# Kernel optimization log

Measured on AMD Instinct MI355X. Metric: run time of the kernel, lower is better.

The kernel has to match this reference:

```python
import jax, jax.numpy as jnp
import numpy as np

D_MODEL = 1024
N_HEADS = 16
DEPTH = D_MODEL // N_HEADS


def setup_inputs() -> dict:
    key = jax.random.key(0)
    ks = jax.random.split(key, 11)
    B, S = 2, 2048
    s = 1.0 / np.sqrt(D_MODEL)
    return {
        "query": jax.random.normal(ks[0], (B, S, D_MODEL), jnp.float32),
        "key": jax.random.normal(ks[1], (B, S, D_MODEL), jnp.float32),
        "value": jax.random.normal(ks[2], (B, S, D_MODEL), jnp.float32),
        "Wq": jax.random.normal(ks[3], (D_MODEL, D_MODEL), jnp.float32) * s,
        "bq": jnp.zeros((D_MODEL,), jnp.float32),
        "Wk": jax.random.normal(ks[4], (D_MODEL, D_MODEL), jnp.float32) * s,
        "bk": jnp.zeros((D_MODEL,), jnp.float32),
        "Wv": jax.random.normal(ks[5], (D_MODEL, D_MODEL), jnp.float32) * s,
        "bv": jnp.zeros((D_MODEL,), jnp.float32),
        "Wo": jax.random.normal(ks[6], (D_MODEL, D_MODEL), jnp.float32) * s,
        "bo": jnp.zeros((D_MODEL,), jnp.float32),
    }


def _split_heads(x):
    B, S, _ = x.shape
    return x.reshape(B, S, N_HEADS, DEPTH).transpose(0, 2, 1, 3)  # [B,H,S,depth]


def reference(query, key, value, Wq, bq, Wk, bk, Wv, bv, Wo, bo):
    q = _split_heads(query @ Wq.T + bq)   # [B,H,S,d]
    k = _split_heads(key @ Wk.T + bk)
    v = _split_heads(value @ Wv.T + bv)
    scale = 1.0 / jnp.sqrt(jnp.asarray(DEPTH, jnp.float32))
    scores = jnp.einsum('bhqd,bhkd->bhqk', q, k) * scale  # [B,H,S,S]
    attn = jax.nn.softmax(scores, axis=-1)
    ctx = jnp.einsum('bhqk,bhkd->bhqd', attn, v)          # [B,H,S,d]
    B, H, S, d = ctx.shape
    ctx = ctx.transpose(0, 2, 1, 3).reshape(B, S, D_MODEL)
    out = ctx @ Wo.T + bo
    return out, attn
```

## Files before the change

### kernel.cpp

```cpp
#include <hip/hip_runtime.h>
#include <stdint.h>


#define DEV __device__ __forceinline__

typedef __attribute__((ext_vector_type(8))) short short8;
typedef __attribute__((ext_vector_type(4))) short short4v;
typedef __attribute__((ext_vector_type(4))) float f32x4;
typedef __attribute__((ext_vector_type(4))) uint32_t u32x4;

DEV short f2bf(float f) {
  uint32_t u = __builtin_bit_cast(uint32_t, f);
  u += 0x7fffu + ((u >> 16) & 1u);
  return (short)(u >> 16);
}

DEV uint32_t cvtpk_bf16(float a, float b) {
  uint32_t r;
  asm("v_cvt_pk_bf16_f32 %0, %1, %2" : "=v"(r) : "v"(a), "v"(b));
  return r;
}

DEV void gload_lds16(const void* g, void* l) {
  __builtin_amdgcn_global_load_lds(
      (const __attribute__((address_space(1))) void*)g,
      (__attribute__((address_space(3))) void*)l,
      16, 0, 0);
}

__global__ __launch_bounds__(256) void attn_fused(
    const short* __restrict__ q, const short* __restrict__ k,
    const short* __restrict__ vT, float* __restrict__ attn,
    short* __restrict__ ctx) {
  __shared__ __align__(16) char Ps[4 * 32 * 128];

  const int tid = threadIdx.x;
  const int lane = tid & 63;
  const int wm = tid >> 6;
  const int c = lane & 15;
  const int g = lane >> 4;
  const int orig = blockIdx.x;
  const int sid = (orig & 7) * 64 + (orig >> 3);
  const int qb = sid & 15;
  const int z = sid >> 4;

  const short* qz = q + (size_t)z * 131072 + (size_t)(qb * 128 + wm * 32) * 64;
  const short* kz = k + (size_t)z * 131072;
  const short* vz = vT + (size_t)z * 131072;
  float* az = attn + (size_t)z * 4194304 + (size_t)(qb * 128 + wm * 32) * 2048;

  short8 qf[2][2];
#pragma unroll
  for (int m = 0; m < 2; ++m)
#pragma unroll
    for (int kk = 0; kk < 2; ++kk)
      qf[m][kk] = *(const short8*)(qz + (m * 16 + c) * 64 + kk * 32 + g * 8);

  float l_part[2][4];
#pragma unroll
  for (int m = 0; m < 2; ++m)
#pragma unroll
    for (int j = 0; j < 4; ++j) l_part[m][j] = 0.f;

  for (int kt = 0; kt < 16; ++kt) {
    const short* kzt = kz + kt * 8192;
    f32x4 s[2][8];
#pragma unroll
    for (int m = 0; m < 2; ++m)
#pragma unroll
      for (int n = 0; n < 8; ++n) s[m][n] = f32x4{0.f, 0.f, 0.f, 0.f};
#pragma unroll
    for (int kk = 0; kk < 2; ++kk) {
#pragma unroll
      for (int n = 0; n < 8; ++n) {
        const short8 bf =
            *(const short8*)(kzt + (n * 16 + c) * 64 + kk * 32 + g * 8);
        s[0][n] = __builtin_amdgcn_mfma_f32_16x16x32_bf16(qf[0][kk], bf,
                                                          s[0][n], 0, 0, 0);
        s[1][n] = __builtin_amdgcn_mfma_f32_16x16x32_bf16(qf[1][kk], bf,
                                                          s[1][n], 0, 0, 0);
      }
    }
#pragma unroll
    for (int m = 0; m < 2; ++m)
#pragma unroll
      for (int j = 0; j < 4; ++j)
#pragma unroll
        for (int n = 0; n < 8; ++n) l_part[m][j] += __expf(s[m][n][j]);
  }

  float inv_l[2][4];
#pragma unroll
  for (int m = 0; m < 2; ++m)
#pragma unroll
    for (int j = 0; j < 4; ++j) {
      float l = l_part[m][j];
      l += __shfl_xor(l, 1, 64);
      l += __shfl_xor(l, 2, 64);
      l += __shfl_xor(l, 4, 64);
      l += __shfl_xor(l, 8, 64);
      inv_l[m][j] = 1.0f / l;
    }

  f32x4 o[2][4];
#pragma unroll
  for (int m = 0; m < 2; ++m)
#pragma unroll
    for (int n = 0; n < 4; ++n) o[m][n] = f32x4{0.f, 0.f, 0.f, 0.f};

  char* Pw = Ps + wm * 4096;

  for (int kt = 0; kt < 16; ++kt) {
    const short* kzt = kz + kt * 8192;
    f32x4 s[2][8];
#pragma unroll
    for (int m = 0; m < 2; ++m)
#pragma unroll
      for (int n = 0; n < 8; ++n) s[m][n] = f32x4{0.f, 0.f, 0.f, 0.f};
#pragma unroll
    for (int kk = 0; kk < 2; ++kk) {
#pragma unroll
      for (int n = 0; n < 8; ++n) {
        const short8 bf =
            *(const short8*)(kzt + (n * 16 + c) * 64 + kk * 32 + g * 8);
        s[0][n] = __builtin_amdgcn_mfma_f32_16x16x32_bf16(qf[0][kk], bf,
                                                          s[0][n], 0, 0, 0);
        s[1][n] = __builtin_amdgcn_mfma_f32_16x16x32_bf16(qf[1][kk], bf,
                                                          s[1][n], 0, 0, 0);
      }
    }
#pragma unroll
    for (int m = 0; m < 2; ++m)
#pragma unroll
      for (int j = 0; j < 4; ++j) {
        const float il = inv_l[m][j];
#pragma unroll
        for (int n = 0; n < 8; ++n) s[m][n][j] = __expf(s[m][n][j]) * il;
      }
#pragma unroll
    for (int m = 0; m < 2; ++m)
#pragma unroll
      for (int n = 0; n < 8; ++n)
#pragma unroll
        for (int j = 0; j < 4; ++j)
          __builtin_nontemporal_store(
              s[m][n][j], az + (size_t)(m * 16 + g * 4 + j) * 2048 +
                              kt * 128 + n * 16 + c);
#pragma unroll
    for (int kc = 0; kc < 4; ++kc) {
#pragma unroll
      for (int m = 0; m < 2; ++m)
#pragma unroll
        for (int nn = 0; nn < 2; ++nn)
#pragma unroll
          for (int j = 0; j < 4; ++j) {
            const int r = m * 16 + g * 4 + j;
            *(float*)(Pw + r * 128 +
                      (((nn * 16 + c) * 4) ^ ((r & 7) << 4))) =
                s[m][kc * 2 + nn][j];
          }
      short8 paf[2];
#pragma unroll
      for (int m = 0; m < 2; ++m) {
        const int r = m * 16 + c;
        const int X = (r & 7) << 4;
        const f32x4 lo = *(const f32x4*)(Pw + r * 128 + ((g * 32) ^ X));
        const f32x4 hi = *(const f32x4*)(Pw + r * 128 + ((g * 32 + 16) ^ X));
        u32x4 pk;
        pk[0] = cvtpk_bf16(lo[0], lo[1]);
        pk[1] = cvtpk_bf16(lo[2], lo[3]);
        pk[2] = cvtpk_bf16(hi[0], hi[1]);
        pk[3] = cvtpk_bf16(hi[2], hi[3]);
        paf[m] = __builtin_bit_cast(short8, pk);
      }
#pragma unroll
      for (int n2 = 0; n2 < 4; ++n2) {
        const short8 vf = *(const short8*)(vz + (size_t)(n2 * 16 + c) * 2048 +
                                           kt * 128 + kc * 32 + g * 8);
        o[0][n2] = __builtin_amdgcn_mfma_f32_16x16x32_bf16(paf[0], vf,
                                                           o[0][n2], 0, 0, 0);
        o[1][n2] = __builtin_amdgcn_mfma_f32_16x16x32_bf16(paf[1], vf,
                                                           o[1][n2], 0, 0, 0);
      }
    }
  }

  const int b = z >> 4, h = z & 15;
#pragma unroll
  for (int m = 0; m < 2; ++m)
#pragma unroll
    for (int n2 = 0; n2 < 4; ++n2)
#pragma unroll
      for (int j = 0; j < 4; ++j)
        ctx[((size_t)(b * 2048 + qb * 128 + wm * 32 + m * 16 + g * 4 + j)) *
                1024 + h * 64 + n2 * 16 + c] = f2bf(o[m][n2][j]);
}

enum { M_PROJ = 0, M_OUT = 3 };

struct GP {
  const void* A0; const void* A1; const void* A2;
  const short* B;
  const float* b0; const float* b1; const float* b2;
  void* C;
  int lda, ldb, K;
  long aBS, bBS;
};

template<int WM, int WN, int AM, int AN, bool CONVA, int MODE>
__global__ __launch_bounds__(256) void gemm_nt(GP p) {
  constexpr int BM = WM * 16 * AM;
  constexpr int BN = WN * 16 * AN;
  static_assert(WM * WN == 4, "4 waves / 256 threads");
  __shared__ __align__(16) char As[BM * 128];
  __shared__ __align__(16) char Bs[BN * 128];

  const int tid = threadIdx.x;
  const int lane = tid & 63;
  const int z = blockIdx.y;
  const int orig = blockIdx.x;
  const int sid = (orig & 7) * 32 + (orig >> 3);
  const int bm0 = (sid >> 3) * BM;
  const int bn0 = (sid & 7) * BN;

  const void* Aroot; const float* bias;
  if constexpr (MODE == M_PROJ) {
    Aroot = (z == 0) ? p.A0 : (z == 1 ? p.A1 : p.A2);
    bias  = (z == 0) ? p.b0 : (z == 1 ? p.b1 : p.b2);
  } else {
    Aroot = p.A0; bias = p.b0;
  }

  f32x4 acc[AM][AN];
#pragma unroll
  for (int m = 0; m < AM; ++m)
#pragma unroll
    for (int n = 0; n < AN; ++n) acc[m][n] = f32x4{0.f, 0.f, 0.f, 0.f};

  const int wave = tid >> 6;
  const int wm = wave / WN;
  const int wn = wave % WN;

  const int nK = p.K >> 6;
  for (int kt = 0; kt < nK; ++kt) {
    if constexpr (CONVA) {
      const float* Af = (const float*)Aroot + (size_t)z * p.aBS +
                        (size_t)bm0 * p.lda + kt * 64;
#pragma unroll
      for (int sw = 0; sw < BM / 16; ++sw) {
        const int r = sw * 16 + (tid >> 4);
        const int s8 = tid & 15;
        const float4 v = *(const float4*)(Af + (size_t)r * p.lda + s8 * 4);
        short4v oo;
        oo[0] = f2bf(v.x); oo[1] = f2bf(v.y); oo[2] = f2bf(v.z); oo[3] = f2bf(v.w);
        const int boff = (r * 128 + s8 * 8) ^ ((r & 7) << 4);
        *(short4v*)(As + boff) = oo;
      }
    } else {
      const short* Ab = (const short*)Aroot + (size_t)z * p.aBS +
                        (size_t)bm0 * p.lda + kt * 64;
#pragma unroll
      for (int sw = 0; sw < BM / 32; ++sw) {
        const int r = sw * 32 + (tid >> 3);
        const int c8 = (tid & 7) ^ (r & 7);
        gload_lds16(Ab + (size_t)r * p.lda + c8 * 8, As + (sw * 256 + tid) * 16);
      }
    }
    {
      const short* Bb = p.B + (size_t)z * p.bBS + (size_t)bn0 * p.ldb + kt * 64;
#pragma unroll
      for (int sw = 0; sw < BN / 32; ++sw) {
        const int r = sw * 32 + (tid >> 3);
        const int c8 = (tid & 7) ^ (r & 7);
        gload_lds16(Bb + (size_t)r * p.ldb + c8 * 8, Bs + (sw * 256 + tid) * 16);
      }
    }
    __syncthreads();
#pragma unroll
    for (int kk = 0; kk < 2; ++kk) {
      const int kb = kk * 64 + (lane >> 4) * 16;
      short8 aF[AM], bF[AN];
#pragma unroll
      for (int m = 0; m < AM; ++m) {
        const int r = wm * (16 * AM) + m * 16 + (lane & 15);
        aF[m] = *(const short8*)(As + ((r * 128 + kb) ^ ((r & 7) << 4)));
      }
#pragma unroll
      for (int n = 0; n < AN; ++n) {
        const int r = wn * (16 * AN) + n * 16 + (lane & 15);
        bF[n] = *(const short8*)(Bs + ((r * 128 + kb) ^ ((r & 7) << 4)));
      }
#pragma unroll
      for (int m = 0; m < AM; ++m)
#pragma unroll
        for (int n = 0; n < AN; ++n)
          acc[m][n] = __builtin_amdgcn_mfma_f32_16x16x32_bf16(
              aF[m], bF[n], acc[m][n], 0, 0, 0);
    }
    __syncthreads();
  }

#pragma unroll
  for (int m = 0; m < AM; ++m) {
#pragma unroll
    for (int n = 0; n < AN; ++n) {
#pragma unroll
      for (int j = 0; j < 4; ++j) {
        const int gm = bm0 + wm * (16 * AM) + m * 16 + ((lane >> 4) << 2) + j;
        const int gn = bn0 + wn * (16 * AN) + n * 16 + (lane & 15);
        const float v = acc[m][n][j];
        if constexpr (MODE == M_PROJ) {
          float vb = v + bias[gn];
          if (z == 0) vb *= 0.125f;
          const int b = gm >> 11, s = gm & 2047;
          const int h = gn >> 6, d = gn & 63;
          short* C = (short*)p.C;
          if (z < 2) {
            C[(size_t)z * 4194304 + (((size_t)(b * 16 + h) * 2048 + s) * 64 + d)] = f2bf(vb);
          } else {
            C[(size_t)2 * 4194304 + (((size_t)(b * 16 + h) * 64 + d) * 2048 + s)] = f2bf(vb);
          }
        } else {
          __builtin_nontemporal_store(
              v + bias[gn], (float*)p.C + (size_t)gm * 1024 + gn);
        }
      }
    }
  }
}

__global__ __launch_bounds__(256) void cvt_w(const float* w0, const float* w1,
                                             const float* w2, const float* w3,
                                             short* out) {
  const float* w = (blockIdx.y == 0) ? w0 : (blockIdx.y == 1) ? w1
                 : (blockIdx.y == 2) ? w2 : w3;
  short* o = out + (size_t)blockIdx.y * 1048576;
  const int i = (blockIdx.x * 256 + threadIdx.x) * 4;
  const float4 v = *(const float4*)(w + i);
  short4v s;
  s[0] = f2bf(v.x); s[1] = f2bf(v.y); s[2] = f2bf(v.z); s[3] = f2bf(v.w);
  *(short4v*)(o + i) = s;
}

extern "C" void kernel_launch(void* const* d_in, const int* in_sizes, int n_in,
                              void* d_out, int out_size, void* d_ws, size_t ws_size,
                              hipStream_t stream) {
  const float* query = (const float*)d_in[0];
  const float* key_  = (const float*)d_in[1];
  const float* value = (const float*)d_in[2];
  const float* Wq = (const float*)d_in[3];
  const float* bq = (const float*)d_in[4];
  const float* Wk = (const float*)d_in[5];
  const float* bk = (const float*)d_in[6];
  const float* Wv = (const float*)d_in[7];
  const float* bv = (const float*)d_in[8];
  const float* Wo = (const float*)d_in[9];
  const float* bo = (const float*)d_in[10];

  float* out  = (float*)d_out;
  float* attn = (float*)d_out + 4194304;

  short* ws   = (short*)d_ws;
  short* Wb   = ws;
  short* qkv  = ws + 4194304;
  short* ctx  = ws + 4 * 4194304;

  cvt_w<<<dim3(1024, 4), 256, 0, stream>>>(Wq, Wk, Wv, Wo, Wb);

  {
    GP p{};
    p.A0 = query; p.A1 = key_; p.A2 = value;
    p.B = Wb; p.b0 = bq; p.b1 = bk; p.b2 = bv;
    p.C = qkv;
    p.lda = 1024; p.ldb = 1024; p.K = 1024;
    p.aBS = 0; p.bBS = 1048576;
    gemm_nt<2, 2, 4, 4, true, M_PROJ><<<dim3(256, 3), 256, 0, stream>>>(p);
  }

  attn_fused<<<dim3(512), 256, 0, stream>>>(
      qkv, qkv + 4194304, qkv + 2 * 4194304, attn, ctx);

  {
    GP p{};
    p.A0 = ctx;
    p.B = Wb + 3 * 1048576;
    p.b0 = bo;
    p.C = out;
    p.lda = 1024; p.ldb = 1024; p.K = 1024;
    p.aBS = 0; p.bBS = 0;
    gemm_nt<2, 2, 4, 4, false, M_OUT><<<dim3(256, 1), 256, 0, stream>>>(p);
  }
}
```

Measured before the change: 315.6 us.

## Stage K/V tiles in LDS, vectorize attn stores, pre-convert activations to bf16

The attention kernel now stages each K tile (and the V^T tile) into swizzled shared memory with async global-to-LDS loads, so the four waves share them instead of each reading from global memory. Barriers are added around each tile. The attention-probability stores move to after the LDS transpose so they go out as 16-byte nontemporal vector stores rather than scalar stores. When the workspace is large enough, a new pre-pass converts the query, key and value activations to bf16 so the projection GEMM can skip in-loop fp32 conversion, at the cost of an extra read and write pass over the activations.

```diff
diff --git a/kernel.cpp b/kernel.cpp
--- a/kernel.cpp
+++ b/kernel.cpp
@@ -28,10 +28,27 @@
       16, 0, 0);
 }
 
+template<int UNITS, int SPR>
+DEV void stage_swz(const short* src, int stride, char* lds, int tid) {
+#pragma unroll
+  for (int i = 0; i < UNITS; ++i) {
+    const int u = tid + i * 256;
+    const int r = u / SPR;
+    const int s = (u % SPR) ^ (r & 7);
+    gload_lds16(src + (size_t)r * stride + s * 8, lds + u * 16);
+  }
+}
+
+DEV short8 ldsfrag(const char* lds, int row, int kbyte, int rowb) {
+  return *(const short8*)(lds + row * rowb + (kbyte ^ ((row & 7) << 4)));
+}
+
 __global__ __launch_bounds__(256) void attn_fused(
     const short* __restrict__ q, const short* __restrict__ k,
     const short* __restrict__ vT, float* __restrict__ attn,
     short* __restrict__ ctx) {
+  __shared__ __align__(16) char Ks[128 * 128];
+  __shared__ __align__(16) char Vs[64 * 256];
   __shared__ __align__(16) char Ps[4 * 32 * 128];
 
   const int tid = threadIdx.x;
@@ -63,7 +80,9 @@
     for (int j = 0; j < 4; ++j) l_part[m][j] = 0.f;
 
   for (int kt = 0; kt < 16; ++kt) {
-    const short* kzt = kz + kt * 8192;
+    if (kt) __syncthreads();
+    stage_swz<4, 8>(kz + kt * 8192, 64, Ks, tid);
+    __syncthreads();
     f32x4 s[2][8];
 #pragma unroll
     for (int m = 0; m < 2; ++m)
@@ -73,8 +92,7 @@
     for (int kk = 0; kk < 2; ++kk) {
 #pragma unroll
       for (int n = 0; n < 8; ++n) {
-        const short8 bf =
-            *(const short8*)(kzt + (n * 16 + c) * 64 + kk * 32 + g * 8);
+        const short8 bf = ldsfrag(Ks, n * 16 + c, kk * 64 + g * 16, 128);
         s[0][n] = __builtin_amdgcn_mfma_f32_16x16x32_bf16(qf[0][kk], bf,
                                                           s[0][n], 0, 0, 0);
         s[1][n] = __builtin_amdgcn_mfma_f32_16x16x32_bf16(qf[1][kk], bf,
@@ -111,7 +129,10 @@
   char* Pw = Ps + wm * 4096;
 
   for (int kt = 0; kt < 16; ++kt) {
-    const short* kzt = kz + kt * 8192;
+    __syncthreads();
+    stage_swz<4, 8>(kz + kt * 8192, 64, Ks, tid);
+    stage_swz<4, 16>(vz + kt * 128, 2048, Vs, tid);
+    __syncthreads();
     f32x4 s[2][8];
 #pragma unroll
     for (int m = 0; m < 2; ++m)
@@ -121,8 +142,7 @@
     for (int kk = 0; kk < 2; ++kk) {
 #pragma unroll
       for (int n = 0; n < 8; ++n) {
-        const short8 bf =
-            *(const short8*)(kzt + (n * 16 + c) * 64 + kk * 32 + g * 8);
+        const short8 bf = ldsfrag(Ks, n * 16 + c, kk * 64 + g * 16, 128);
         s[0][n] = __builtin_amdgcn_mfma_f32_16x16x32_bf16(qf[0][kk], bf,
                                                           s[0][n], 0, 0, 0);
         s[1][n] = __builtin_amdgcn_mfma_f32_16x16x32_bf16(qf[1][kk], bf,
@@ -137,15 +157,6 @@
 #pragma unroll
         for (int n = 0; n < 8; ++n) s[m][n][j] = __expf(s[m][n][j]) * il;
       }
-#pragma unroll
-    for (int m = 0; m < 2; ++m)
-#pragma unroll
-      for (int n = 0; n < 8; ++n)
-#pragma unroll
-        for (int j = 0; j < 4; ++j)
-          __builtin_nontemporal_store(
-              s[m][n][j], az + (size_t)(m * 16 + g * 4 + j) * 2048 +
-                              kt * 128 + n * 16 + c);
 #pragma unroll
     for (int kc = 0; kc < 4; ++kc) {
 #pragma unroll
@@ -166,6 +177,9 @@
         const int X = (r & 7) << 4;
         const f32x4 lo = *(const f32x4*)(Pw + r * 128 + ((g * 32) ^ X));
         const f32x4 hi = *(const f32x4*)(Pw + r * 128 + ((g * 32 + 16) ^ X));
+        float* dst = az + (size_t)r * 2048 + kt * 128 + kc * 32 + g * 8;
+        __builtin_nontemporal_store(lo, (f32x4*)dst);
+        __builtin_nontemporal_store(hi, (f32x4*)(dst + 4));
         u32x4 pk;
         pk[0] = cvtpk_bf16(lo[0], lo[1]);
         pk[1] = cvtpk_bf16(lo[2], lo[3]);
@@ -175,8 +189,7 @@
       }
 #pragma unroll
       for (int n2 = 0; n2 < 4; ++n2) {
-        const short8 vf = *(const short8*)(vz + (size_t)(n2 * 16 + c) * 2048 +
-                                           kt * 128 + kc * 32 + g * 8);
+        const short8 vf = ldsfrag(Vs, n2 * 16 + c, kc * 64 + g * 16, 256);
         o[0][n2] = __builtin_amdgcn_mfma_f32_16x16x32_bf16(paf[0], vf,
                                                            o[0][n2], 0, 0, 0);
         o[1][n2] = __builtin_amdgcn_mfma_f32_16x16x32_bf16(paf[1], vf,
@@ -225,8 +238,11 @@
 
   const void* Aroot; const float* bias;
   if constexpr (MODE == M_PROJ) {
-    Aroot = (z == 0) ? p.A0 : (z == 1 ? p.A1 : p.A2);
-    bias  = (z == 0) ? p.b0 : (z == 1 ? p.b1 : p.b2);
+    if constexpr (CONVA)
+      Aroot = (z == 0) ? p.A0 : (z == 1 ? p.A1 : p.A2);
+    else
+      Aroot = p.A0;
+    bias = (z == 0) ? p.b0 : (z == 1 ? p.b1 : p.b2);
   } else {
     Aroot = p.A0; bias = p.b0;
   }
@@ -329,6 +345,26 @@
   }
 }
 
+__global__ __launch_bounds__(256) void cvt_all(
+    const float* q, const float* k, const float* v, const float* w0,
+    const float* w1, const float* w2, const float* w3, short* xb, short* Wb) {
+  const int y = blockIdx.y;
+  const float* src; short* dst; int n;
+  if (y < 3) {
+    src = (y == 0) ? q : (y == 1) ? k : v;
+    dst = xb + (size_t)y * 4194304; n = 4194304;
+  } else {
+    src = (y == 3) ? w0 : (y == 4) ? w1 : (y == 5) ? w2 : w3;
+    dst = Wb + (size_t)(y - 3) * 1048576; n = 1048576;
+  }
+  const int i = (blockIdx.x * 256 + threadIdx.x) * 4;
+  if (i >= n) return;
+  const float4 val = *(const float4*)(src + i);
+  short4v s;
+  s[0] = f2bf(val.x); s[1] = f2bf(val.y); s[2] = f2bf(val.z); s[3] = f2bf(val.w);
+  *(short4v*)(dst + i) = s;
+}
+
 __global__ __launch_bounds__(256) void cvt_w(const float* w0, const float* w1,
                                              const float* w2, const float* w3,
                                              short* out) {
@@ -359,35 +395,65 @@
 
   float* out  = (float*)d_out;
   float* attn = (float*)d_out + 4194304;
-
   short* ws   = (short*)d_ws;
-  short* Wb   = ws;
-  short* qkv  = ws + 4194304;
-  short* ctx  = ws + 4 * 4194304;
-
-  cvt_w<<<dim3(1024, 4), 256, 0, stream>>>(Wq, Wk, Wv, Wo, Wb);
-
-  {
-    GP p{};
-    p.A0 = query; p.A1 = key_; p.A2 = value;
-    p.B = Wb; p.b0 = bq; p.b1 = bk; p.b2 = bv;
-    p.C = qkv;
-    p.lda = 1024; p.ldb = 1024; p.K = 1024;
-    p.aBS = 0; p.bBS = 1048576;
-    gemm_nt<2, 2, 4, 4, true, M_PROJ><<<dim3(256, 3), 256, 0, stream>>>(p);
-  }
-
-  attn_fused<<<dim3(512), 256, 0, stream>>>(
-      qkv, qkv + 4194304, qkv + 2 * 4194304, attn, ctx);
-
-  {
-    GP p{};
-    p.A0 = ctx;
-    p.B = Wb + 3 * 1048576;
-    p.b0 = bo;
-    p.C = out;
-    p.lda = 1024; p.ldb = 1024; p.K = 1024;
-    p.aBS = 0; p.bBS = 0;
-    gemm_nt<2, 2, 4, 4, false, M_OUT><<<dim3(256, 1), 256, 0, stream>>>(p);
-  }
-}
+
+  const bool big_ws = ws_size >= (size_t)64 * 1024 * 1024;
+
+  if (big_ws) {
+    short* xb  = ws;
+    short* Wb  = ws + 3 * 4194304;
+    short* qkv = ws + 3 * 4194304 + 4 * 1048576;
+    short* ctx = qkv + 3 * 4194304;
+
+    cvt_all<<<dim3(4096, 7), 256, 0, stream>>>(query, key_, value, Wq, Wk, Wv,
+                                               Wo, xb, Wb);
+    {
+      GP p{};
+      p.A0 = xb;
+      p.B = Wb; p.b0 = bq; p.b1 = bk; p.b2 = bv;
+      p.C = qkv;
+      p.lda = 1024; p.ldb = 1024; p.K = 1024;
+      p.aBS = 4194304; p.bBS = 1048576;
+      gemm_nt<2, 2, 4, 4, false, M_PROJ><<<dim3(256, 3), 256, 0, stream>>>(p);
+    }
+    attn_fused<<<dim3(512), 256, 0, stream>>>(
+        qkv, qkv + 4194304, qkv + 2 * 4194304, attn, ctx);
+    {
+      GP p{};
+      p.A0 = ctx;
+      p.B = Wb + 3 * 1048576;
+      p.b0 = bo;
+      p.C = out;
+      p.lda = 1024; p.ldb = 1024; p.K = 1024;
+      p.aBS = 0; p.bBS = 0;
+      gemm_nt<2, 2, 4, 4, false, M_OUT><<<dim3(256, 1), 256, 0, stream>>>(p);
+    }
+  } else {
+    short* Wb  = ws;
+    short* qkv = ws + 4194304;
+    short* ctx = ws + 4 * 4194304;
+
+    cvt_w<<<dim3(1024, 4), 256, 0, stream>>>(Wq, Wk, Wv, Wo, Wb);
+    {
+      GP p{};
+      p.A0 = query; p.A1 = key_; p.A2 = value;
+      p.B = Wb; p.b0 = bq; p.b1 = bk; p.b2 = bv;
+      p.C = qkv;
+      p.lda = 1024; p.ldb = 1024; p.K = 1024;
+      p.aBS = 0; p.bBS = 1048576;
+      gemm_nt<2, 2, 4, 4, true, M_PROJ><<<dim3(256, 3), 256, 0, stream>>>(p);
+    }
+    attn_fused<<<dim3(512), 256, 0, stream>>>(
+        qkv, qkv + 4194304, qkv + 2 * 4194304, attn, ctx);
+    {
+      GP p{};
+      p.A0 = ctx;
+      p.B = Wb + 3 * 1048576;
+      p.b0 = bo;
+      p.C = out;
+      p.lda = 1024; p.ldb = 1024; p.K = 1024;
+      p.aBS = 0; p.bBS = 0;
+      gemm_nt<2, 2, 4, 4, false, M_OUT><<<dim3(256, 1), 256, 0, stream>>>(p);
+    }
+  }
+}
```

New measurement: 431.9 us. 36.8% more time.
